# Optimization experiments

Measured on AMD Instinct MI355X. Metric: run time of the kernel, lower is better.

The kernel has to match this reference:

```python
import jax, jax.numpy as jnp
import numpy as np

PAGE_SIZE = 16
HQ, HKV, D = 32, 8, 128   # num_q_heads, num_kv_heads, head_dim
B, S = 8, 1024            # requests, tokens per request (prefill)


def setup_inputs() -> dict:
    key = jax.random.key(0)
    ks = jax.random.split(key, 4)
    T = B * S
    q = jax.random.normal(ks[0], (T, HQ * D), jnp.float32)
    k = jax.random.normal(ks[1], (T, HKV * D), jnp.float32)
    v = jax.random.normal(ks[2], (T, HKV * D), jnp.float32)
    pages_per_seq = S // PAGE_SIZE          # 64
    num_pages = B * pages_per_seq + 64      # 576 (with slack pages)
    # random page assignment: each request owns pages_per_seq distinct pages
    perm = jax.random.permutation(ks[3], num_pages)[: B * pages_per_seq]
    page_table = perm.reshape(B, pages_per_seq).astype(jnp.int32)
    key_buf = jnp.zeros((num_pages * PAGE_SIZE, HKV, D), jnp.float32)
    value_buf = jnp.zeros((num_pages * PAGE_SIZE, HKV, D), jnp.float32)
    return {"q": q, "k": k, "v": v, "key_buf": key_buf,
            "value_buf": value_buf, "page_table": page_table}


def reference(q, k, v, key_buf, value_buf, page_table):
    Bq, P = page_table.shape
    S_ = P * PAGE_SIZE
    T = Bq * S_
    scale = 1.0 / np.sqrt(D).astype(np.float32)

    k3 = k.reshape(T, HKV, D)
    v3 = v.reshape(T, HKV, D)

    # store_kv_cache: scatter new tokens into the paged KV buffers
    # token (b, s) -> slot page_table[b, s//PAGE_SIZE]*PAGE_SIZE + s%PAGE_SIZE
    slots = (page_table[:, :, None] * PAGE_SIZE
             + jnp.arange(PAGE_SIZE, dtype=page_table.dtype)).reshape(-1)  # [T]
    kb = key_buf.at[slots].set(k3)
    vb = value_buf.at[slots].set(v3)

    # prefill attention: gather each request's KV from the paged cache
    K = kb[slots].reshape(Bq, S_, HKV, D)
    V = vb[slots].reshape(Bq, S_, HKV, D)
    Q = q.reshape(Bq, S_, HKV, HQ // HKV, D)  # GQA grouping: g = HQ//HKV

    scores = jnp.einsum('bqhgd,bkhd->bhgqk', Q, K) * scale  # [B,Hkv,g,S,S]
    causal = jnp.tril(jnp.ones((S_, S_), dtype=bool))
    scores = jnp.where(causal, scores, jnp.float32(-1e30))
    p = jax.nn.softmax(scores, axis=-1)
    out = jnp.einsum('bhgqk,bkhd->bqhgd', p, V)  # [B,S,Hkv,g,D]
    return out.reshape(T, HQ * D)
```

## Files before the change

kernel.cpp:

```cpp
#include <hip/hip_runtime.h>

typedef _Float16 f16;
typedef __attribute__((ext_vector_type(8))) _Float16 f16x8;
typedef __attribute__((ext_vector_type(4))) _Float16 f16x4;
typedef __attribute__((ext_vector_type(4))) float f32x4;

constexpr int HQ = 32, HKV = 8, D = 128, NB = 8, S = 1024;
constexpr float SCALE_LOG2E = 0.08838834764831845f * 1.4426950408889634f;

static __device__ __forceinline__ void gload16(const f16* g, f16* l) {
    __builtin_amdgcn_global_load_lds(
        (const __attribute__((address_space(1))) void*)g,
        (__attribute__((address_space(3))) void*)l, 16, 0, 0);
}

__global__ __launch_bounds__(256) void pack_kernel(const float* __restrict__ k,
                                                   const float* __restrict__ v,
                                                   f16* __restrict__ kf,
                                                   f16* __restrict__ vf) {
    __shared__ __attribute__((aligned(16))) f16 tile[64][136];
    int blk = blockIdx.x;
    int tl = blk & 15, hk = (blk >> 4) & 7, b = blk >> 7;
    int t = threadIdx.x;
    size_t cbase = ((size_t)(b * 8 + hk) * 16 + tl) * 1024;

    const float* kin = k + ((size_t)(b * S + tl * 64) * HKV + hk) * D;
#pragma unroll
    for (int i = 0; i < 8; i++) {
        int flat = t + 256 * i;
        int row = flat >> 5, c4 = flat & 31;
        float4 x = *(const float4*)(kin + (size_t)row * (HKV * D) + c4 * 4);
        *(f16x4*)&tile[row][c4 * 4] = (f16x4){ (f16)x.x,(f16)x.y,(f16)x.z,(f16)x.w };
    }
    __syncthreads();
#pragma unroll
    for (int i = 0; i < 4; i++) {
        int c_loc = t + 256 * i;
        int mb = c_loc >> 8, kb = (c_loc >> 6) & 3, lane = c_loc & 63;
        int quad = lane >> 4, lq = lane & 15;
        f16x8 o = *(const f16x8*)&tile[mb * 16 + lq][kb * 32 + quad * 8];
        *(f16x8*)(kf + (cbase + c_loc) * 8) = o;
    }
    __syncthreads();

    const float* vin = v + ((size_t)(b * S + tl * 64) * HKV + hk) * D;
#pragma unroll
    for (int i = 0; i < 8; i++) {
        int flat = t + 256 * i;
        int row = flat >> 5, c4 = flat & 31;
        float4 x = *(const float4*)(vin + (size_t)row * (HKV * D) + c4 * 4);
        *(f16x4*)&tile[row][c4 * 4] = (f16x4){ (f16)x.x,(f16)x.y,(f16)x.z,(f16)x.w };
    }
    __syncthreads();
#pragma unroll
    for (int i = 0; i < 4; i++) {
        int c_loc = t + 256 * i;
        int mi = c_loc >> 7, ks2 = (c_loc >> 6) & 1, lane = c_loc & 63;
        int quad = lane >> 4, lq = lane & 15;
        int d = mi * 16 + lq;
        f16 buf[8];
#pragma unroll
        for (int o = 0; o < 2; o++)
#pragma unroll
            for (int j = 0; j < 4; j++)
                buf[o * 4 + j] = tile[ks2 * 32 + o * 16 + quad * 4 + j][d];
        *(f16x8*)(vf + (cbase + c_loc) * 8) = *(const f16x8*)buf;
    }
}

__global__ __launch_bounds__(256, 2) void attn_kernel(
    const float* __restrict__ q, const f16* __restrict__ kf,
    const f16* __restrict__ vf, float* __restrict__ out) {

    __shared__ f16 ldsK[2][64 * 128];
    __shared__ f16 ldsV[2][64 * 128];

    int id = blockIdx.x;
    int xcd = id & 7;
    int slot = id >> 3;
    int gl = slot >> 5;
    int inner = slot & 31;
    int g = gl * 8 + xcd;
    int b = g >> 3, hk = g & 7;
    int hq = (hk << 2) | (inner & 3);
    int qt = 7 - (((inner >> 2) + gl) & 7);

    int t = threadIdx.x;
    int w = t >> 6, lane = t & 63, quad = lane >> 4, lq = lane & 15;
    int qwb = qt * 128 + w * 32;

    const f16* kfb = kf + (size_t)(b * 8 + hk) * (S * D);
    const f16* vfb = vf + (size_t)(b * 8 + hk) * (S * D);

    int nt = qwb / 64 + 1;
    int ntmax = qt * 2 + 2;

#pragma unroll
    for (int i = 0; i < 4; i++) {
        int sl = w * 4 + i;
        gload16(kfb + (size_t)(sl * 64 + lane) * 8, &ldsK[0][sl * 512]);
        gload16(vfb + (size_t)(sl * 64 + lane) * 8, &ldsV[0][sl * 512]);
    }

    f16x8 qf[2][4];
#pragma unroll
    for (int nq = 0; nq < 2; nq++) {
        int qg = qwb + nq * 16 + lq;
        const float* qp = q + ((size_t)(b * S + qg) * HQ + hq) * D + quad * 8;
#pragma unroll
        for (int kb = 0; kb < 4; kb++) {
            float4 x = *(const float4*)(qp + kb * 32);
            float4 y = *(const float4*)(qp + kb * 32 + 4);
            qf[nq][kb] = (f16x8){
                (f16)(x.x * SCALE_LOG2E), (f16)(x.y * SCALE_LOG2E),
                (f16)(x.z * SCALE_LOG2E), (f16)(x.w * SCALE_LOG2E),
                (f16)(y.x * SCALE_LOG2E), (f16)(y.y * SCALE_LOG2E),
                (f16)(y.z * SCALE_LOG2E), (f16)(y.w * SCALE_LOG2E) };
        }
    }

    f32x4 zero4 = { 0.f, 0.f, 0.f, 0.f };
    f32x4 oacc[8][2];
#pragma unroll
    for (int mi = 0; mi < 8; mi++) { oacc[mi][0] = zero4; oacc[mi][1] = zero4; }
    float m_i[2] = { -1e30f, -1e30f };
    float l_i[2] = { 0.f, 0.f };

    __syncthreads();

    int cur = 0;
    for (int kt = 0; kt < ntmax; kt++) {
        if (kt + 1 < ntmax) {
            const f16* kn = kfb + (size_t)(kt + 1) * (64 * 128);
            const f16* vn = vfb + (size_t)(kt + 1) * (64 * 128);
#pragma unroll
            for (int i = 0; i < 4; i++) {
                int sl = w * 4 + i;
                gload16(kn + (size_t)(sl * 64 + lane) * 8, &ldsK[cur ^ 1][sl * 512]);
                gload16(vn + (size_t)(sl * 64 + lane) * 8, &ldsV[cur ^ 1][sl * 512]);
            }
        }

        if (kt < nt) {
            f32x4 sacc[4][2];
#pragma unroll
            for (int mb = 0; mb < 4; mb++) { sacc[mb][0] = zero4; sacc[mb][1] = zero4; }
            __builtin_amdgcn_s_setprio(1);
#pragma unroll
            for (int mb = 0; mb < 4; mb++) {
#pragma unroll
                for (int kb = 0; kb < 4; kb++) {
                    f16x8 af = *(const f16x8*)&ldsK[cur][((mb * 4 + kb) * 64 + lane) * 8];
                    sacc[mb][0] = __builtin_amdgcn_mfma_f32_16x16x32_f16(af, qf[0][kb], sacc[mb][0], 0, 0, 0);
                    sacc[mb][1] = __builtin_amdgcn_mfma_f32_16x16x32_f16(af, qf[1][kb], sacc[mb][1], 0, 0, 0);
                }
            }
            __builtin_amdgcn_s_setprio(0);

            bool diag = (kt == nt - 1);
            f16x4 pf[4][2];
#pragma unroll
            for (int nq = 0; nq < 2; nq++) {
                float mt = -1e30f;
                if (diag) {
                    int qg = qwb + nq * 16 + lq;
#pragma unroll
                    for (int mb = 0; mb < 4; mb++)
#pragma unroll
                        for (int r4 = 0; r4 < 4; r4++) {
                            float vs = sacc[mb][nq][r4];
                            int key = kt * 64 + mb * 16 + quad * 4 + r4;
                            vs = (key <= qg) ? vs : -1e30f;
                            sacc[mb][nq][r4] = vs;
                            mt = fmaxf(mt, vs);
                        }
                } else {
#pragma unroll
                    for (int mb = 0; mb < 4; mb++)
#pragma unroll
                        for (int r4 = 0; r4 < 4; r4++)
                            mt = fmaxf(mt, sacc[mb][nq][r4]);
                }
                mt = fmaxf(mt, __shfl_xor(mt, 16, 64));
                mt = fmaxf(mt, __shfl_xor(mt, 32, 64));
                float mnew = m_i[nq];
                if (!__all(mt <= mnew + 8.0f)) {
                    mnew = fmaxf(mnew, mt);
                    float a = exp2f(m_i[nq] - mnew);
                    m_i[nq] = mnew;
                    l_i[nq] *= a;
#pragma unroll
                    for (int mi = 0; mi < 8; mi++) oacc[mi][nq] = oacc[mi][nq] * a;
                }
                float ls = 0.f;
#pragma unroll
                for (int mb = 0; mb < 4; mb++) {
#pragma unroll
                    for (int r4 = 0; r4 < 4; r4++) {
                        float e = exp2f(sacc[mb][nq][r4] - mnew);
                        sacc[mb][nq][r4] = e;
                        ls += e;
                    }
                    auto lo = __builtin_amdgcn_cvt_pkrtz(sacc[mb][nq][0], sacc[mb][nq][1]);
                    auto hi = __builtin_amdgcn_cvt_pkrtz(sacc[mb][nq][2], sacc[mb][nq][3]);
                    pf[mb][nq] = (f16x4){ (f16)lo[0], (f16)lo[1], (f16)hi[0], (f16)hi[1] };
                }
                ls += __shfl_xor(ls, 16, 64);
                ls += __shfl_xor(ls, 32, 64);
                l_i[nq] += ls;
            }

            __builtin_amdgcn_s_setprio(1);
#pragma unroll
            for (int mi = 0; mi < 8; mi++) {
#pragma unroll
                for (int ks2 = 0; ks2 < 2; ks2++) {
                    f16x8 vv = *(const f16x8*)&ldsV[cur][((mi * 2 + ks2) * 64 + lane) * 8];
                    f16x4 v0 = { vv[0], vv[1], vv[2], vv[3] };
                    f16x4 v1 = { vv[4], vv[5], vv[6], vv[7] };
                    oacc[mi][0] = __builtin_amdgcn_mfma_f32_16x16x16f16(v0, pf[ks2 * 2 + 0][0], oacc[mi][0], 0, 0, 0);
                    oacc[mi][0] = __builtin_amdgcn_mfma_f32_16x16x16f16(v1, pf[ks2 * 2 + 1][0], oacc[mi][0], 0, 0, 0);
                    oacc[mi][1] = __builtin_amdgcn_mfma_f32_16x16x16f16(v0, pf[ks2 * 2 + 0][1], oacc[mi][1], 0, 0, 0);
                    oacc[mi][1] = __builtin_amdgcn_mfma_f32_16x16x16f16(v1, pf[ks2 * 2 + 1][1], oacc[mi][1], 0, 0, 0);
                }
            }
            __builtin_amdgcn_s_setprio(0);
        }

        __syncthreads();
        cur ^= 1;
    }

#pragma unroll
    for (int nq = 0; nq < 2; nq++) {
        float linv = 1.0f / l_i[nq];
        int qg = qwb + nq * 16 + lq;
        float* op = out + ((size_t)(b * S + qg) * HQ + hq) * D + quad * 4;
#pragma unroll
        for (int mi = 0; mi < 8; mi++) {
            float4 vv = { oacc[mi][nq][0] * linv, oacc[mi][nq][1] * linv,
                          oacc[mi][nq][2] * linv, oacc[mi][nq][3] * linv };
            *(float4*)(op + mi * 16) = vv;
        }
    }
}

extern "C" void kernel_launch(void* const* d_in, const int* in_sizes, int n_in,
                              void* d_out, int out_size, void* d_ws, size_t ws_size,
                              hipStream_t stream) {
    (void)in_sizes; (void)n_in; (void)out_size; (void)ws_size;
    const float* q = (const float*)d_in[0];
    const float* k = (const float*)d_in[1];
    const float* v = (const float*)d_in[2];
    float* out = (float*)d_out;

    f16* kf = (f16*)d_ws;
    f16* vf = kf + (size_t)NB * HKV * S * D;

    pack_kernel<<<1024, 256, 0, stream>>>(k, v, kf, vf);
    attn_kernel<<<NB * HQ * 8, 256, 0, stream>>>(q, kf, vf, out);
}
```

Baseline: 409.0 us.

## Single-buffer K/V in LDS with staggered loads to raise occupancy

Replaces the double-buffered K and V LDS tiles with single buffers, halving shared memory from 64KB to 32KB per block, and raises the launch-bounds occupancy hint from 2 to 4 blocks per CU. To keep some overlap, the next K tile is loaded after QK^T finishes, overlapping the softmax and PV step, and the next V tile is loaded after PV, overlapping the next QK^T. This adds a second barrier per iteration. The higher occupancy hint also tightens the register budget, which could cause spills given the large accumulator arrays.

Result: slower. 754.2 us (+84.4%).

```diff
diff --git a/kernel.cpp b/kernel.cpp
--- a/kernel.cpp
+++ b/kernel.cpp
@@ -68,12 +68,12 @@
     }
 }
 
-__global__ __launch_bounds__(256, 2) void attn_kernel(
+__global__ __launch_bounds__(256, 4) void attn_kernel(
     const float* __restrict__ q, const f16* __restrict__ kf,
     const f16* __restrict__ vf, float* __restrict__ out) {
 
-    __shared__ f16 ldsK[2][64 * 128];
-    __shared__ f16 ldsV[2][64 * 128];
+    __shared__ f16 ldsK[64 * 128];
+    __shared__ f16 ldsV[64 * 128];
 
     int id = blockIdx.x;
     int xcd = id & 7;
@@ -97,9 +97,9 @@
 
 #pragma unroll
     for (int i = 0; i < 4; i++) {
-        int sl = w * 4 + i;
-        gload16(kfb + (size_t)(sl * 64 + lane) * 8, &ldsK[0][sl * 512]);
-        gload16(vfb + (size_t)(sl * 64 + lane) * 8, &ldsV[0][sl * 512]);
+        int si = w * 4 + i;
+        gload16(kfb + (size_t)(si * 64 + lane) * 8, &ldsK[si * 512]);
+        gload16(vfb + (size_t)(si * 64 + lane) * 8, &ldsV[si * 512]);
     }
 
     f16x8 qf[2][4];
@@ -128,37 +128,40 @@
 
     __syncthreads();
 
-    int cur = 0;
     for (int kt = 0; kt < ntmax; kt++) {
+        bool live = (kt < nt);
+        bool diag = (kt == nt - 1);
+        f32x4 sacc[4][2];
+        f16x4 pf[4][2];
+
+        if (live) {
+#pragma unroll
+            for (int mb = 0; mb < 4; mb++) { sacc[mb][0] = zero4; sacc[mb][1] = zero4; }
+            __builtin_amdgcn_s_setprio(1);
+#pragma unroll
+            for (int mb = 0; mb < 4; mb++) {
+#pragma unroll
+                for (int kb = 0; kb < 4; kb++) {
+                    f16x8 af = *(const f16x8*)&ldsK[((mb * 4 + kb) * 64 + lane) * 8];
+                    sacc[mb][0] = __builtin_amdgcn_mfma_f32_16x16x32_f16(af, qf[0][kb], sacc[mb][0], 0, 0, 0);
+                    sacc[mb][1] = __builtin_amdgcn_mfma_f32_16x16x32_f16(af, qf[1][kb], sacc[mb][1], 0, 0, 0);
+                }
+            }
+            __builtin_amdgcn_s_setprio(0);
+        }
+
+        __syncthreads();
+
         if (kt + 1 < ntmax) {
             const f16* kn = kfb + (size_t)(kt + 1) * (64 * 128);
-            const f16* vn = vfb + (size_t)(kt + 1) * (64 * 128);
 #pragma unroll
             for (int i = 0; i < 4; i++) {
-                int sl = w * 4 + i;
-                gload16(kn + (size_t)(sl * 64 + lane) * 8, &ldsK[cur ^ 1][sl * 512]);
-                gload16(vn + (size_t)(sl * 64 + lane) * 8, &ldsV[cur ^ 1][sl * 512]);
-            }
-        }
-
-        if (kt < nt) {
-            f32x4 sacc[4][2];
-#pragma unroll
-            for (int mb = 0; mb < 4; mb++) { sacc[mb][0] = zero4; sacc[mb][1] = zero4; }
-            __builtin_amdgcn_s_setprio(1);
-#pragma unroll
-            for (int mb = 0; mb < 4; mb++) {
-#pragma unroll
-                for (int kb = 0; kb < 4; kb++) {
-                    f16x8 af = *(const f16x8*)&ldsK[cur][((mb * 4 + kb) * 64 + lane) * 8];
-                    sacc[mb][0] = __builtin_amdgcn_mfma_f32_16x16x32_f16(af, qf[0][kb], sacc[mb][0], 0, 0, 0);
-                    sacc[mb][1] = __builtin_amdgcn_mfma_f32_16x16x32_f16(af, qf[1][kb], sacc[mb][1], 0, 0, 0);
-                }
-            }
-            __builtin_amdgcn_s_setprio(0);
-
-            bool diag = (kt == nt - 1);
-            f16x4 pf[4][2];
+                int si = w * 4 + i;
+                gload16(kn + (size_t)(si * 64 + lane) * 8, &ldsK[si * 512]);
+            }
+        }
+
+        if (live) {
 #pragma unroll
             for (int nq = 0; nq < 2; nq++) {
                 float mt = -1e30f;
@@ -215,7 +218,7 @@
             for (int mi = 0; mi < 8; mi++) {
 #pragma unroll
                 for (int ks2 = 0; ks2 < 2; ks2++) {
-                    f16x8 vv = *(const f16x8*)&ldsV[cur][((mi * 2 + ks2) * 64 + lane) * 8];
+                    f16x8 vv = *(const f16x8*)&ldsV[((mi * 2 + ks2) * 64 + lane) * 8];
                     f16x4 v0 = { vv[0], vv[1], vv[2], vv[3] };
                     f16x4 v1 = { vv[4], vv[5], vv[6], vv[7] };
                     oacc[mi][0] = __builtin_amdgcn_mfma_f32_16x16x16f16(v0, pf[ks2 * 2 + 0][0], oacc[mi][0], 0, 0, 0);
@@ -228,7 +231,15 @@
         }
 
         __syncthreads();
-        cur ^= 1;
+
+        if (kt + 1 < ntmax) {
+            const f16* vn = vfb + (size_t)(kt + 1) * (64 * 128);
+#pragma unroll
+            for (int i = 0; i < 4; i++) {
+                int si = w * 4 + i;
+                gload16(vn + (size_t)(si * 64 + lane) * 8, &ldsV[si * 512]);
+            }
+        }
     }
 
 #pragma unroll
```
